# Optimization experiments

Measured on AMD Instinct MI355X. Metric: run time of the kernel, lower is better.

## Reference

```python
import jax, jax.numpy as jnp
import numpy as np

RADIUS = 0.1
NSAMPLE = 32


def _ball_query(radius, nsample, xyz, new_xyz):
    # xyz: (B,N,3), new_xyz: (B,npoint,3) -> idx (B,npoint,nsample) int32
    # Faithful to the CUDA ball_query: take the first nsample in-radius indices
    # (in ascending point order); pad with the first found index.
    N = xyz.shape[1]
    d2 = jnp.sum((new_xyz[:, :, None, :] - xyz[:, None, :, :]) ** 2, axis=-1)  # (B,np,N)
    mask = d2 < radius * radius
    key_arr = jnp.where(mask, jnp.arange(N, dtype=jnp.int32), jnp.int32(N))
    idx = jnp.sort(key_arr, axis=-1)[..., :nsample]  # (B,np,ns)
    first = idx[..., :1]
    idx = jnp.where(idx == N, first, idx)
    idx = jnp.where(idx == N, 0, idx)  # empty-ball fallback (matches zero-init buffer)
    return idx


def _group(features, idx):
    # features (B,C,N), idx (B,np,ns) -> (B,C,np,ns)
    return jax.vmap(lambda f, i: f[:, i])(features, idx)


def _forward(xyz, new_xyz):
    idx = jax.lax.stop_gradient(_ball_query(RADIUS, NSAMPLE, xyz, new_xyz))
    xyz_t = jnp.transpose(xyz, (0, 2, 1))                 # (B,3,N)
    g = _group(xyz_t, idx)                                # (B,3,np,ns) grouped_xyz
    c = jnp.transpose(new_xyz, (0, 2, 1))[..., None]      # (B,3,np,1)  new_xyz_reshaped

    # pairwise distances within each group
    diff = g[..., :, None] - g[..., None, :]              # (B,3,np,ns,ns)
    dis = jnp.sqrt(jnp.sum(diff * diff, axis=1))          # (B,np,ns,ns)
    mean_dis = jnp.mean(dis, axis=3)                      # (B,np,ns)
    tip_idx = jnp.argmax(mean_dis, axis=2)                # (B,np)
    tip_pts = jnp.take_along_axis(g, tip_idx[:, None, :, None], axis=3)[..., 0]  # (B,3,np)

    cb = jnp.broadcast_to(c, g.shape)                     # (B,3,np,ns)
    gpv = jnp.cross(jnp.cross(cb, g, axis=1), cb, axis=1)
    gpv = gpv / jnp.linalg.norm(gpv, axis=1)[:, None]     # (B,3,np,ns)

    new_r = jnp.sqrt(jnp.sum(c * c, axis=1))              # (B,np,1)
    new_norm = c / (new_r[:, None] + 1e-8)                # (B,3,np,1)

    c3 = c[..., 0]                                        # (B,3,np)
    tpv = jnp.cross(jnp.cross(c3, tip_pts, axis=1), c3, axis=1)
    tpv = tpv / jnp.linalg.norm(tpv, axis=1)[:, None]     # (B,3,np)

    gcv = jnp.cross(gpv, jnp.broadcast_to(tpv[..., None], gpv.shape), axis=1)
    sinv = jnp.sum(gcv * new_norm, axis=1)                # (B,np,ns)

    dis_t = jnp.transpose(dis, (0, 2, 1, 3))              # (B,ns,np,ns)
    dis_sort = jnp.sort(dis_t, axis=1) * sinv[:, None]    # (B,ns,np,ns)
    grouped_r = jnp.sqrt(jnp.sum(g * g, axis=1))          # (B,np,ns)
    return jnp.concatenate([dis_sort, grouped_r[:, None]], axis=1)  # (B,ns+1,np,ns)


def setup_inputs() -> dict:
    key = jax.random.key(0)
    k1, k2 = jax.random.split(key)
    xyz = jax.random.uniform(k1, (4, 16384, 3), dtype=jnp.float32)
    new_xyz = jax.random.uniform(k2, (4, 2048, 3), dtype=jnp.float32)
    return {"xyz": xyz, "new_xyz": new_xyz}


def reference(xyz, new_xyz):
    return _forward(xyz, new_xyz)
```

## Files before the change

### kernel.cpp

```cpp
#include <hip/hip_runtime.h>


#define BB 4
#define NN 16384
#define MM 2048
#define NS 32
#define R2 0.01f
#define GZ 20
#define NCELL 2000
#define CPAD 2048
#define HCAP 128

#define WS_PTS_OFF (96 * 1024)
#define WS_NEED (WS_PTS_OFF + (size_t)BB * NN * 16)

__device__ __forceinline__ int cell_of(float x, float y, float z) {
    int ci = (int)(x * 10.0f); ci = ci < 0 ? 0 : (ci > 9 ? 9 : ci);
    int cj = (int)(y * 10.0f); cj = cj < 0 ? 0 : (cj > 9 ? 9 : cj);
    int ck = (int)(z * 20.0f); ck = ck < 0 ? 0 : (ck > 19 ? 19 : ck);
    return (ci * 10 + cj) * GZ + ck;
}

__global__ __launch_bounds__(1024) void k_build_part(const float* __restrict__ xyz,
                                                     int* __restrict__ off,
                                                     float4* __restrict__ pts) {
    __shared__ int hist[CPAD];
    __shared__ int wsum[16];

    const int b = blockIdx.x >> 5;
    const int r = blockIdx.x & 31;
    const int t = threadIdx.x;
    const int lane = t & 63, wid = t >> 6;
    const float4* __restrict__ xb4 = (const float4*)(xyz + (size_t)b * NN * 3);
    float4* __restrict__ ptsb = pts + (size_t)b * NN;

    hist[t] = 0;
    hist[t + 1024] = 0;
    __syncthreads();

    #pragma unroll
    for (int it = 0; it < 4; ++it) {
        const int f = (it * 1024 + t) * 3;
        float4 a = xb4[f];
        float4 g = xb4[f + 1];
        float4 c = xb4[f + 2];
        atomicAdd(&hist[cell_of(a.x, a.y, a.z)], 1);
        atomicAdd(&hist[cell_of(a.w, g.x, g.y)], 1);
        atomicAdd(&hist[cell_of(g.z, g.w, c.x)], 1);
        atomicAdd(&hist[cell_of(c.y, c.z, c.w)], 1);
    }
    __syncthreads();

    const int v0 = hist[2 * t];
    const int v1 = hist[2 * t + 1];
    const int s = v0 + v1;
    int xs = s;
    #pragma unroll
    for (int o = 1; o < 64; o <<= 1) {
        int u = __shfl_up(xs, o);
        if (lane >= o) xs += u;
    }
    if (lane == 63) wsum[wid] = xs;
    __syncthreads();
    int pre = 0;
    #pragma unroll
    for (int i2 = 0; i2 < 16; ++i2) pre += (i2 < wid) ? wsum[i2] : 0;
    const int excl = pre + xs - s;
    hist[2 * t] = excl;
    hist[2 * t + 1] = excl + v0;
    if (r == 0) {
        off[b * CPAD + 2 * t] = excl;
        off[b * CPAD + 2 * t + 1] = excl + v0;
    }
    __syncthreads();

    const int clo = r * 64, chi = clo + 64;
    #pragma unroll
    for (int it = 0; it < 4; ++it) {
        const int f = (it * 1024 + t) * 3;
        float4 a = xb4[f];
        float4 g = xb4[f + 1];
        float4 c = xb4[f + 2];
        const int i0 = (it * 1024 + t) * 4;
        float X[4] = {a.x, a.w, g.z, c.y};
        float Y[4] = {a.y, g.x, g.w, c.z};
        float Z[4] = {a.z, g.y, c.x, c.w};
        #pragma unroll
        for (int k = 0; k < 4; ++k) {
            int cc = cell_of(X[k], Y[k], Z[k]);
            if (cc >= clo && cc < chi) {
                int pos = atomicAdd(&hist[cc], 1);
                ptsb[pos] = make_float4(X[k], Y[k], Z[k], __int_as_float(i0 + k));
            }
        }
    }
}

__global__ __launch_bounds__(256) void qgr_grid_kernel(
    const float* __restrict__ xyz,
    const float* __restrict__ nxyz,
    const int* __restrict__ offi,
    const float4* __restrict__ pts,
    float* __restrict__ out) {

    __shared__ float4 s_hit[4][2][HCAP];
    __shared__ float4 s_sel[4][2][NS];

    const int lane = threadIdx.x & 63;
    const int w = threadIdx.x >> 6;
    const int sub = lane & 31;
    const int half = lane >> 5;
    const int q0 = blockIdx.x * 8 + w * 2;
    const int b = q0 >> 11;

    const float* xb = xyz + (size_t)b * NN * 3;
    const float* nq = nxyz + (size_t)q0 * 3;
    const float cx0 = nq[0], cy0 = nq[1], cz0 = nq[2];
    const float cx1 = nq[3], cy1 = nq[4], cz1 = nq[5];
    const unsigned long long lmask = (1ull << lane) - 1ull;

    const int* offb = offi + b * CPAD;
    const float4* ptsb = pts + (size_t)b * NN;

    int hits01[2];
    for (int tq = 0; tq < 2; ++tq) {
        const float ccx = tq ? cx1 : cx0;
        const float ccy = tq ? cy1 : cy0;
        const float ccz = tq ? cz1 : cz0;

        int ci0 = (int)(ccx * 10.0f); ci0 = ci0 < 0 ? 0 : (ci0 > 9 ? 9 : ci0);
        int cj0 = (int)(ccy * 10.0f); cj0 = cj0 < 0 ? 0 : (cj0 > 9 ? 9 : cj0);
        int ck0 = (int)(ccz * 20.0f); ck0 = ck0 < 0 ? 0 : (ck0 > 19 ? 19 : ck0);
        int zlo = ck0 > 2 ? ck0 - 2 : 0;
        int zhi = ck0 < 17 ? ck0 + 2 : 19;

        int rs[9], rl[9];
        #pragma unroll
        for (int r = 0; r < 9; ++r) { rs[r] = 0; rl[r] = 0; }
        int nr = 0;
        #pragma unroll
        for (int di = -1; di <= 1; ++di) {
            int ii = ci0 + di; if ((unsigned)ii > 9u) continue;
            #pragma unroll
            for (int dj = -1; dj <= 1; ++dj) {
                int jj = cj0 + dj; if ((unsigned)jj > 9u) continue;
                int base2 = (ii * 10 + jj) * GZ;
                int s0 = offb[base2 + zlo];
                int e0 = offb[base2 + zhi + 1];
                int len = e0 - s0;
                if (len > 0) { rs[nr] = s0; rl[nr] = len; ++nr; }
            }
        }

        float4 P[9];
        #pragma unroll
        for (int r = 0; r < 9; ++r) {
            int a = (lane < rl[r]) ? (rs[r] + lane) : 0;
            P[r] = ptsb[a];
        }

        int hits = 0;
        #pragma unroll
        for (int r = 0; r < 9; ++r) {
            float dx = __fsub_rn(ccx, P[r].x);
            float dy = __fsub_rn(ccy, P[r].y);
            float dz = __fsub_rn(ccz, P[r].z);
            float d2 = __fadd_rn(__fadd_rn(__fmul_rn(dx, dx), __fmul_rn(dy, dy)),
                                 __fmul_rn(dz, dz));
            bool hit = (lane < rl[r]) && (d2 < R2);
            unsigned long long bal = __ballot(hit);
            if (bal) {
                int rank = __popcll(bal & lmask);
                int slot = hits + rank;
                if (hit && slot < HCAP) s_hit[w][tq][slot] = P[r];
                hits += __popcll(bal);
            }
        }
        for (int r = 0; r < nr; ++r) {
            for (int t0 = 64; t0 < rl[r]; t0 += 64) {
                int t = t0 + lane;
                bool act = t < rl[r];
                float4 Q = ptsb[rs[r] + (act ? t : 0)];
                float dx = __fsub_rn(ccx, Q.x);
                float dy = __fsub_rn(ccy, Q.y);
                float dz = __fsub_rn(ccz, Q.z);
                float d2 = __fadd_rn(__fadd_rn(__fmul_rn(dx, dx), __fmul_rn(dy, dy)),
                                     __fmul_rn(dz, dz));
                bool hit = act && (d2 < R2);
                unsigned long long bal = __ballot(hit);
                if (bal) {
                    int rank = __popcll(bal & lmask);
                    int slot = hits + rank;
                    if (hit && slot < HCAP) s_hit[w][tq][slot] = Q;
                    hits += __popcll(bal);
                }
            }
        }
        hits01[tq] = hits;
    }

    const int hits = half ? hits01[1] : hits01[0];
    const int cap = hits < HCAP ? hits : HCAP;
    const float ccx = half ? cx1 : cx0;
    const float ccy = half ? cy1 : cy0;
    const float ccz = half ? cz1 : cz0;

    int key[4];
    #pragma unroll
    for (int r = 0; r < 4; ++r) {
        int e = r * 32 + sub;
        int idx_e = __float_as_int(s_hit[w][half][e].w);
        key[r] = (e < cap) ? ((idx_e << 8) | e) : 0x7fffffff;
    }

    #pragma unroll
    for (int k = 2; k <= 16; k <<= 1) {
        #pragma unroll
        for (int j = k >> 1; j > 0; j >>= 1) {
            bool lower = (sub & j) == 0;
            bool asc = (sub & k) == 0;
            bool keepmin = (lower == asc);
            #pragma unroll
            for (int r = 0; r < 4; ++r) {
                int p = __shfl_xor(key[r], j);
                key[r] = keepmin ? min(key[r], p) : max(key[r], p);
            }
        }
    }
    #pragma unroll
    for (int j = 16; j > 0; j >>= 1) {
        bool lower = (sub & j) == 0;
        #pragma unroll
        for (int r = 0; r < 4; ++r) {
            int p = __shfl_xor(key[r], j);
            bool asc = (r & 1) == 0;
            key[r] = (lower == asc) ? min(key[r], p) : max(key[r], p);
        }
    }
    {
        int t0 = min(key[0], key[1]); key[1] = max(key[0], key[1]); key[0] = t0;
        int t2 = max(key[2], key[3]); key[3] = min(key[2], key[3]); key[2] = t2;
    }
    #pragma unroll
    for (int j = 16; j > 0; j >>= 1) {
        bool lower = (sub & j) == 0;
        #pragma unroll
        for (int r = 0; r < 4; ++r) {
            int p = __shfl_xor(key[r], j);
            bool asc = (r & 2) == 0;
            key[r] = (lower == asc) ? min(key[r], p) : max(key[r], p);
        }
    }
    {
        int t0 = min(key[0], key[2]); key[2] = max(key[0], key[2]); key[0] = t0;
        int t1 = min(key[1], key[3]); key[3] = max(key[1], key[3]); key[1] = t1;
        t0 = min(key[0], key[1]); key[1] = max(key[0], key[1]); key[0] = t0;
        t1 = min(key[2], key[3]); key[3] = max(key[2], key[3]); key[2] = t1;
    }
    #pragma unroll
    for (int j = 16; j > 0; j >>= 1) {
        bool lower = (sub & j) == 0;
        #pragma unroll
        for (int r = 0; r < 4; ++r) {
            int p = __shfl_xor(key[r], j);
            key[r] = lower ? min(key[r], p) : max(key[r], p);
        }
    }

    const int found = hits < NS ? hits : NS;
    const int hbase = half << 5;
    float4 sel = make_float4(0.f, 0.f, 0.f, 0.f);
    if (sub < found) sel = s_hit[w][half][key[0] & 0xFF];
    float p0x, p0y, p0z;
    if (found == 0) { p0x = xb[0]; p0y = xb[1]; p0z = xb[2]; }
    else {
        p0x = __shfl(sel.x, hbase); p0y = __shfl(sel.y, hbase); p0z = __shfl(sel.z, hbase);
    }
    if (sub >= found) { sel.x = p0x; sel.y = p0y; sel.z = p0z; }
    const float hx = sel.x, hy = sel.y, hz = sel.z;

    s_sel[w][half][sub] = sel;

    float v[NS];
    #pragma unroll
    for (int ii = 0; ii < NS; ++ii) {
        float4 B = s_sel[w][half][ii];
        float dx = __fsub_rn(B.x, hx);
        float dy = __fsub_rn(B.y, hy);
        float dz = __fsub_rn(B.z, hz);
        v[ii] = sqrtf(__fadd_rn(__fadd_rn(__fmul_rn(dx, dx), __fmul_rn(dy, dy)),
                                __fmul_rn(dz, dz)));
    }

    float r8[8];
    #pragma unroll
    for (int t = 0; t < 8; ++t) {
        r8[t] = __fadd_rn(__fadd_rn(__fadd_rn(v[t], v[t + 8]), v[t + 16]), v[t + 24]);
    }
    float mv = __fadd_rn(__fadd_rn(__fadd_rn(r8[0], r8[1]), __fadd_rn(r8[2], r8[3])),
                         __fadd_rn(__fadd_rn(r8[4], r8[5]), __fadd_rn(r8[6], r8[7])));
    int mi = sub;
    #pragma unroll
    for (int off = 1; off < 32; off <<= 1) {
        float ov = __shfl_xor(mv, off);
        int oi = __shfl_xor(mi, off);
        if (ov > mv || (ov == mv && oi < mi)) { mv = ov; mi = oi; }
    }

    float4 T = s_sel[w][half][mi];
    const float tx = T.x, ty = T.y, tz = T.z;

    float ux = ccy * tz - ccz * ty, uy = ccz * tx - ccx * tz, uz = ccx * ty - ccy * tx;
    float vx = uy * ccz - uz * ccy, vy = uz * ccx - ux * ccz, vz = ux * ccy - uy * ccx;
    float vn = fmaxf(sqrtf(vx * vx + vy * vy + vz * vz), 1e-37f);
    float tnx = vx / vn, tny = vy / vn, tnz = vz / vn;

    float nrm = sqrtf(ccx * ccx + ccy * ccy + ccz * ccz);
    float dn = nrm + 1e-8f;
    float nnx = ccx / dn, nny = ccy / dn, nnz = ccz / dn;

    float ax = ccy * hz - ccz * hy, ay = ccz * hx - ccx * hz, az = ccx * hy - ccy * hx;
    float px = ay * ccz - az * ccy, py = az * ccx - ax * ccz, pz = ax * ccy - ay * ccx;
    float pn = fmaxf(sqrtf(px * px + py * py + pz * pz), 1e-37f);
    px /= pn; py /= pn; pz /= pn;

    float qx = py * tnz - pz * tny;
    float qy = pz * tnx - px * tnz;
    float qz = px * tny - py * tnx;
    float sinv = qx * nnx + qy * nny + qz * nnz;

    float gr = sqrtf(hx * hx + hy * hy + hz * hz);

    const int m_h = (q0 + half) & (MM - 1);
    const size_t rowstride = (size_t)MM * NS;
    const size_t obase = (((size_t)b * 33) * MM + m_h) * NS + sub;
    out[obase + 32 * rowstride] = gr;

    #pragma unroll
    for (int p = 1; p < NS; p <<= 1) {
        #pragma unroll
        for (int k = p; k >= 1; k >>= 1) {
            #pragma unroll
            for (int j = k & (p - 1); j + k < NS; j += 2 * k) {
                #pragma unroll
                for (int i = 0; i < k; ++i) {
                    if (i + j + k < NS) {
                        int x = i + j, y = i + j + k;
                        if ((x / (2 * p)) == (y / (2 * p))) {
                            float lo = fminf(v[x], v[y]);
                            v[y] = fmaxf(v[x], v[y]);
                            v[x] = lo;
                        }
                    }
                }
            }
        }
    }

    #pragma unroll
    for (int ii = 0; ii < NS; ++ii)
        out[obase + (size_t)ii * rowstride] = v[ii] * sinv;
}

#define CHUNKS 4
__global__ __launch_bounds__(256) void qgr_kernel(
    const float* __restrict__ xyz,
    const float* __restrict__ nxyz,
    float* __restrict__ out) {

    __shared__ float s_gx[4][NS], s_gy[4][NS], s_gz[4][NS];
    __shared__ float s_dis[4][NS][NS + 1];

    const int lane = threadIdx.x & 63;
    const int w = threadIdx.x >> 6;
    const int q = blockIdx.x * 4 + w;
    const int b = q >> 11;
    const int m = q & (MM - 1);

    const float* xb = xyz + (size_t)b * NN * 3;
    const float* nq = nxyz + (size_t)q * 3;
    const float cx = nq[0], cy = nq[1], cz = nq[2];
    const unsigned long long lmask = (1ull << lane) - 1ull;

    int cnt = 0;
    for (int base = 0; base < NN; base += 64 * CHUNKS) {
        float X[CHUNKS], Y[CHUNKS], Z[CHUNKS];
        #pragma unroll
        for (int c = 0; c < CHUNKS; ++c) {
            const float* p = xb + (size_t)(base + c * 64 + lane) * 3;
            X[c] = p[0]; Y[c] = p[1]; Z[c] = p[2];
        }
        bool in[CHUNKS];
        #pragma unroll
        for (int c = 0; c < CHUNKS; ++c) {
            float dx = __fsub_rn(cx, X[c]);
            float dy = __fsub_rn(cy, Y[c]);
            float dz = __fsub_rn(cz, Z[c]);
            float d2 = __fadd_rn(__fadd_rn(__fmul_rn(dx, dx), __fmul_rn(dy, dy)),
                                 __fmul_rn(dz, dz));
            in[c] = d2 < R2;
        }
        #pragma unroll
        for (int c = 0; c < CHUNKS; ++c) {
            unsigned long long bal = __ballot(in[c]);
            if (bal) {
                int rank = __popcll(bal & lmask);
                int slot = cnt + rank;
                if (in[c] && slot < NS) {
                    s_gx[w][slot] = X[c]; s_gy[w][slot] = Y[c]; s_gz[w][slot] = Z[c];
                }
                cnt += __popcll(bal);
            }
        }
        if (cnt >= NS) break;
    }
    __syncthreads();

    int found = cnt < NS ? cnt : NS;
    float p0x, p0y, p0z;
    if (found == 0) { p0x = xb[0]; p0y = xb[1]; p0z = xb[2]; }
    else            { p0x = s_gx[w][0]; p0y = s_gy[w][0]; p0z = s_gz[w][0]; }
    if (lane < NS && lane >= found) {
        s_gx[w][lane] = p0x; s_gy[w][lane] = p0y; s_gz[w][lane] = p0z;
    }
    __syncthreads();

    #pragma unroll
    for (int t = 0; t < 16; ++t) {
        int e = t * 64 + lane;
        int di = e >> 5, dj = e & 31;
        float dx = __fsub_rn(s_gx[w][di], s_gx[w][dj]);
        float dy = __fsub_rn(s_gy[w][di], s_gy[w][dj]);
        float dz = __fsub_rn(s_gz[w][di], s_gz[w][dj]);
        s_dis[w][di][dj] =
            sqrtf(__fadd_rn(__fadd_rn(__fmul_rn(dx, dx), __fmul_rn(dy, dy)), __fmul_rn(dz, dz)));
    }
    __syncthreads();

    {
        int i = lane & 31;
        float r[8];
        #pragma unroll
        for (int t = 0; t < 8; ++t) {
            r[t] = __fadd_rn(__fadd_rn(__fadd_rn(s_dis[w][i][t], s_dis[w][i][t + 8]),
                                        s_dis[w][i][t + 16]),
                             s_dis[w][i][t + 24]);
        }
        float mv = __fadd_rn(__fadd_rn(__fadd_rn(r[0], r[1]), __fadd_rn(r[2], r[3])),
                             __fadd_rn(__fadd_rn(r[4], r[5]), __fadd_rn(r[6], r[7])));
        int mi = i;
        #pragma unroll
        for (int off = 1; off < 64; off <<= 1) {
            float ov = __shfl_xor(mv, off);
            int oi = __shfl_xor(mi, off);
            if (ov > mv || (ov == mv && oi < mi)) { mv = ov; mi = oi; }
        }
        float tx = s_gx[w][mi], ty = s_gy[w][mi], tz = s_gz[w][mi];
        float ux = cy * tz - cz * ty, uy = cz * tx - cx * tz, uz = cx * ty - cy * tx;
        float vx = uy * cz - uz * cy, vy = uz * cx - ux * cz, vz = ux * cy - uy * cx;
        float vn = fmaxf(sqrtf(vx * vx + vy * vy + vz * vz), 1e-37f);
        float tnx = vx / vn, tny = vy / vn, tnz = vz / vn;
        float nr = sqrtf(cx * cx + cy * cy + cz * cz);
        float dn = nr + 1e-8f;
        float nnx = cx / dn, nny = cy / dn, nnz = cz / dn;
        int j = lane & 31;
        float gx = s_gx[w][j], gy = s_gy[w][j], gz = s_gz[w][j];
        float ax = cy * gz - cz * gy, ay = cz * gx - cx * gz, az = cx * gy - cy * gx;
        float px = ay * cz - az * cy, py = az * cx - ax * cz, pz = ax * cy - ay * cx;
        float pn = fmaxf(sqrtf(px * px + py * py + pz * pz), 1e-37f);
        px /= pn; py /= pn; pz /= pn;
        float qx = py * tnz - pz * tny;
        float qy = pz * tnx - px * tnz;
        float qz = px * tny - py * tnx;
        float sinv = qx * nnx + qy * nny + qz * nnz;
        float gr = sqrtf(gx * gx + gy * gy + gz * gz);
        const size_t rowstride = (size_t)MM * NS;
        const size_t obase = (((size_t)b * 33) * MM + m) * NS + j;
        if (lane < NS) out[obase + 32 * rowstride] = gr;
        float v[NS];
        #pragma unroll
        for (int ii = 0; ii < NS; ++ii) v[ii] = s_dis[w][ii][j];
        #pragma unroll
        for (int k = 2; k <= NS; k <<= 1) {
            #pragma unroll
            for (int jj = k >> 1; jj > 0; jj >>= 1) {
                #pragma unroll
                for (int ii = 0; ii < NS; ++ii) {
                    int ll = ii ^ jj;
                    if (ll > ii) {
                        bool up = ((ii & k) == 0);
                        float a = v[ii], c2 = v[ll];
                        bool sw = up ? (a > c2) : (a < c2);
                        if (sw) { v[ii] = c2; v[ll] = a; }
                    }
                }
            }
        }
        if (lane < NS) {
            #pragma unroll
            for (int ii = 0; ii < NS; ++ii)
                out[obase + (size_t)ii * rowstride] = v[ii] * sinv;
        }
    }
}

extern "C" void kernel_launch(void* const* d_in, const int* in_sizes, int n_in,
                              void* d_out, int out_size, void* d_ws, size_t ws_size,
                              hipStream_t stream) {
    (void)in_sizes; (void)n_in; (void)out_size;
    const float* xyz = (const float*)d_in[0];
    const float* nxyz = (const float*)d_in[1];
    float* out = (float*)d_out;

    if (d_ws != nullptr && ws_size >= WS_NEED) {
        char* ws = (char*)d_ws;
        int* off = (int*)ws;
        float4* pts = (float4*)(ws + WS_PTS_OFF);

        k_build_part<<<BB * 32, 1024, 0, stream>>>(xyz, off, pts);
        qgr_grid_kernel<<<(BB * MM) / 8, 256, 0, stream>>>(xyz, nxyz, off, pts, out);
    } else {
        qgr_kernel<<<(BB * MM) / 4, 256, 0, stream>>>(xyz, nxyz, out);
    }
}
```

Before: 96.67 us.

## Split grid build across more blocks and use one query per wavefront

The partition kernel moves from 128 blocks of 1024 threads to 512 blocks of 512 threads, each scattering only 16 cells, so the build spreads across more CUs. The histogram and scan code is adjusted to four cells per thread. The query kernel drops the two-queries-per-wave scheme: each wavefront now handles a single query, and both half-waves compute the same result while only the first half writes it. This removes the serial two-query ball-search loop per wave and the half-wave select logic, but doubles the number of query blocks and wastes half of each wave in the post-processing stage.

```diff
diff --git a/kernel.cpp b/kernel.cpp
--- a/kernel.cpp
+++ b/kernel.cpp
@@ -21,26 +21,26 @@
     return (ci * 10 + cj) * GZ + ck;
 }
 
-__global__ __launch_bounds__(1024) void k_build_part(const float* __restrict__ xyz,
-                                                     int* __restrict__ off,
-                                                     float4* __restrict__ pts) {
+__global__ __launch_bounds__(512) void k_build_part(const float* __restrict__ xyz,
+                                                    int* __restrict__ off,
+                                                    float4* __restrict__ pts) {
     __shared__ int hist[CPAD];
-    __shared__ int wsum[16];
-
-    const int b = blockIdx.x >> 5;
-    const int r = blockIdx.x & 31;
+    __shared__ int wsum[8];
+
+    const int b = blockIdx.x >> 7;
+    const int r = blockIdx.x & 127;
     const int t = threadIdx.x;
     const int lane = t & 63, wid = t >> 6;
     const float4* __restrict__ xb4 = (const float4*)(xyz + (size_t)b * NN * 3);
     float4* __restrict__ ptsb = pts + (size_t)b * NN;
 
-    hist[t] = 0;
-    hist[t + 1024] = 0;
-    __syncthreads();
-
-    #pragma unroll
-    for (int it = 0; it < 4; ++it) {
-        const int f = (it * 1024 + t) * 3;
+    #pragma unroll
+    for (int j = 0; j < 4; ++j) hist[t + j * 512] = 0;
+    __syncthreads();
+
+    #pragma unroll
+    for (int it = 0; it < 8; ++it) {
+        const int f = (it * 512 + t) * 3;
         float4 a = xb4[f];
         float4 g = xb4[f + 1];
         float4 c = xb4[f + 2];
@@ -51,9 +51,10 @@
     }
     __syncthreads();
 
-    const int v0 = hist[2 * t];
-    const int v1 = hist[2 * t + 1];
-    const int s = v0 + v1;
+    const int base = t * 4;
+    int v[4]; int s = 0;
+    #pragma unroll
+    for (int j = 0; j < 4; ++j) { v[j] = hist[base + j]; s += v[j]; }
     int xs = s;
     #pragma unroll
     for (int o = 1; o < 64; o <<= 1) {
@@ -64,24 +65,24 @@
     __syncthreads();
     int pre = 0;
     #pragma unroll
-    for (int i2 = 0; i2 < 16; ++i2) pre += (i2 < wid) ? wsum[i2] : 0;
-    const int excl = pre + xs - s;
-    hist[2 * t] = excl;
-    hist[2 * t + 1] = excl + v0;
-    if (r == 0) {
-        off[b * CPAD + 2 * t] = excl;
-        off[b * CPAD + 2 * t + 1] = excl + v0;
-    }
-    __syncthreads();
-
-    const int clo = r * 64, chi = clo + 64;
-    #pragma unroll
-    for (int it = 0; it < 4; ++it) {
-        const int f = (it * 1024 + t) * 3;
+    for (int i2 = 0; i2 < 8; ++i2) pre += (i2 < wid) ? wsum[i2] : 0;
+    int run = pre + xs - s;
+    #pragma unroll
+    for (int j = 0; j < 4; ++j) {
+        if (r == 0) off[b * CPAD + base + j] = run;
+        hist[base + j] = run;
+        run += v[j];
+    }
+    __syncthreads();
+
+    const int clo = r * 16, chi = clo + 16;
+    #pragma unroll
+    for (int it = 0; it < 8; ++it) {
+        const int f = (it * 512 + t) * 3;
         float4 a = xb4[f];
         float4 g = xb4[f + 1];
         float4 c = xb4[f + 2];
-        const int i0 = (it * 1024 + t) * 4;
+        const int i0 = (it * 512 + t) * 4;
         float X[4] = {a.x, a.w, g.z, c.y};
         float Y[4] = {a.y, g.x, g.w, c.z};
         float Z[4] = {a.z, g.y, c.x, c.w};
@@ -103,31 +104,26 @@
     const float4* __restrict__ pts,
     float* __restrict__ out) {
 
-    __shared__ float4 s_hit[4][2][HCAP];
-    __shared__ float4 s_sel[4][2][NS];
+    __shared__ float4 s_hit[4][HCAP];
+    __shared__ float4 s_sel[4][NS];
 
     const int lane = threadIdx.x & 63;
     const int w = threadIdx.x >> 6;
     const int sub = lane & 31;
     const int half = lane >> 5;
-    const int q0 = blockIdx.x * 8 + w * 2;
-    const int b = q0 >> 11;
+    const int q = blockIdx.x * 4 + w;
+    const int b = q >> 11;
 
     const float* xb = xyz + (size_t)b * NN * 3;
-    const float* nq = nxyz + (size_t)q0 * 3;
-    const float cx0 = nq[0], cy0 = nq[1], cz0 = nq[2];
-    const float cx1 = nq[3], cy1 = nq[4], cz1 = nq[5];
+    const float* nq = nxyz + (size_t)q * 3;
+    const float ccx = nq[0], ccy = nq[1], ccz = nq[2];
     const unsigned long long lmask = (1ull << lane) - 1ull;
 
     const int* offb = offi + b * CPAD;
     const float4* ptsb = pts + (size_t)b * NN;
 
-    int hits01[2];
-    for (int tq = 0; tq < 2; ++tq) {
-        const float ccx = tq ? cx1 : cx0;
-        const float ccy = tq ? cy1 : cy0;
-        const float ccz = tq ? cz1 : cz0;
-
+    int hits = 0;
+    {
         int ci0 = (int)(ccx * 10.0f); ci0 = ci0 < 0 ? 0 : (ci0 > 9 ? 9 : ci0);
         int cj0 = (int)(ccy * 10.0f); cj0 = cj0 < 0 ? 0 : (cj0 > 9 ? 9 : cj0);
         int ck0 = (int)(ccz * 20.0f); ck0 = ck0 < 0 ? 0 : (ck0 > 19 ? 19 : ck0);
@@ -159,7 +155,6 @@
             P[r] = ptsb[a];
         }
 
-        int hits = 0;
         #pragma unroll
         for (int r = 0; r < 9; ++r) {
             float dx = __fsub_rn(ccx, P[r].x);
@@ -172,7 +167,7 @@
             if (bal) {
                 int rank = __popcll(bal & lmask);
                 int slot = hits + rank;
-                if (hit && slot < HCAP) s_hit[w][tq][slot] = P[r];
+                if (hit && slot < HCAP) s_hit[w][slot] = P[r];
                 hits += __popcll(bal);
             }
         }
@@ -191,25 +186,20 @@
                 if (bal) {
                     int rank = __popcll(bal & lmask);
                     int slot = hits + rank;
-                    if (hit && slot < HCAP) s_hit[w][tq][slot] = Q;
+                    if (hit && slot < HCAP) s_hit[w][slot] = Q;
                     hits += __popcll(bal);
                 }
             }
         }
-        hits01[tq] = hits;
-    }
-
-    const int hits = half ? hits01[1] : hits01[0];
+    }
+
     const int cap = hits < HCAP ? hits : HCAP;
-    const float ccx = half ? cx1 : cx0;
-    const float ccy = half ? cy1 : cy0;
-    const float ccz = half ? cz1 : cz0;
 
     int key[4];
     #pragma unroll
     for (int r = 0; r < 4; ++r) {
         int e = r * 32 + sub;
-        int idx_e = __float_as_int(s_hit[w][half][e].w);
+        int idx_e = __float_as_int(s_hit[w][e].w);
         key[r] = (e < cap) ? ((idx_e << 8) | e) : 0x7fffffff;
     }
 
@@ -268,23 +258,24 @@
     }
 
     const int found = hits < NS ? hits : NS;
-    const int hbase = half << 5;
     float4 sel = make_float4(0.f, 0.f, 0.f, 0.f);
-    if (sub < found) sel = s_hit[w][half][key[0] & 0xFF];
+    if (sub < found) sel = s_hit[w][key[0] & 0xFF];
     float p0x, p0y, p0z;
     if (found == 0) { p0x = xb[0]; p0y = xb[1]; p0z = xb[2]; }
     else {
-        p0x = __shfl(sel.x, hbase); p0y = __shfl(sel.y, hbase); p0z = __shfl(sel.z, hbase);
+        p0x = __shfl(sel.x, half << 5);
+        p0y = __shfl(sel.y, half << 5);
+        p0z = __shfl(sel.z, half << 5);
     }
     if (sub >= found) { sel.x = p0x; sel.y = p0y; sel.z = p0z; }
     const float hx = sel.x, hy = sel.y, hz = sel.z;
 
-    s_sel[w][half][sub] = sel;
+    s_sel[w][sub] = sel;
 
     float v[NS];
     #pragma unroll
     for (int ii = 0; ii < NS; ++ii) {
-        float4 B = s_sel[w][half][ii];
+        float4 B = s_sel[w][ii];
         float dx = __fsub_rn(B.x, hx);
         float dy = __fsub_rn(B.y, hy);
         float dz = __fsub_rn(B.z, hz);
@@ -307,7 +298,7 @@
         if (ov > mv || (ov == mv && oi < mi)) { mv = ov; mi = oi; }
     }
 
-    float4 T = s_sel[w][half][mi];
+    float4 T = s_sel[w][mi];
     const float tx = T.x, ty = T.y, tz = T.z;
 
     float ux = ccy * tz - ccz * ty, uy = ccz * tx - ccx * tz, uz = ccx * ty - ccy * tx;
@@ -331,10 +322,10 @@
 
     float gr = sqrtf(hx * hx + hy * hy + hz * hz);
 
-    const int m_h = (q0 + half) & (MM - 1);
+    const int m_h = q & (MM - 1);
     const size_t rowstride = (size_t)MM * NS;
     const size_t obase = (((size_t)b * 33) * MM + m_h) * NS + sub;
-    out[obase + 32 * rowstride] = gr;
+    if (half == 0) out[obase + 32 * rowstride] = gr;
 
     #pragma unroll
     for (int p = 1; p < NS; p <<= 1) {
@@ -357,9 +348,11 @@
         }
     }
 
-    #pragma unroll
-    for (int ii = 0; ii < NS; ++ii)
-        out[obase + (size_t)ii * rowstride] = v[ii] * sinv;
+    if (half == 0) {
+        #pragma unroll
+        for (int ii = 0; ii < NS; ++ii)
+            out[obase + (size_t)ii * rowstride] = v[ii] * sinv;
+    }
 }
 
 #define CHUNKS 4
@@ -517,8 +510,8 @@
         int* off = (int*)ws;
         float4* pts = (float4*)(ws + WS_PTS_OFF);
 
-        k_build_part<<<BB * 32, 1024, 0, stream>>>(xyz, off, pts);
-        qgr_grid_kernel<<<(BB * MM) / 8, 256, 0, stream>>>(xyz, nxyz, off, pts, out);
+        k_build_part<<<512, 512, 0, stream>>>(xyz, off, pts);
+        qgr_grid_kernel<<<(BB * MM) / 4, 256, 0, stream>>>(xyz, nxyz, off, pts, out);
     } else {
         qgr_kernel<<<(BB * MM) / 4, 256, 0, stream>>>(xyz, nxyz, out);
     }
```

New measurement: 108.5 us. 1.12x slower.
